# Optimization experiments

Measured on AMD Instinct MI355X. Metric: run time of the kernel, lower is better.

The kernel has to match this reference:

```python
import jax, jax.numpy as jnp
import numpy as np

B, D, E, H = 2048, 1024, 16, 4096
NUM_ACTIVE = 2
LN_EPS = 1e-5
NORM_EPS = 1e-12


def setup_inputs() -> dict:
    key = jax.random.key(0)
    ks = jax.random.split(key, 4)
    s1 = 1.0 / np.sqrt(D)
    s2 = 1.0 / np.sqrt(H)
    return {
        "input": jax.random.normal(ks[0], (B, D), jnp.float32),
        "ln_gamma": jnp.ones((D,), jnp.float32),
        "ln_beta": jnp.zeros((D,), jnp.float32),
        "expert_keys": jax.random.normal(ks[1], (D, E), jnp.float32),
        "W1": jax.random.normal(ks[2], (E, D, H), jnp.float32) * s1,
        "b1": jnp.zeros((E, H), jnp.float32),
        "W2": jax.random.normal(ks[3], (E, H, D), jnp.float32) * s2,
        "b2": jnp.zeros((E, D), jnp.float32),
    }


def reference(input, ln_gamma, ln_beta, expert_keys, W1, b1, W2, b2):
    # Gating: LayerNorm(input) @ normalize(expert_keys, dim=-1)
    mu = jnp.mean(input, axis=-1, keepdims=True)
    var = jnp.mean((input - mu) ** 2, axis=-1, keepdims=True)
    xn = (input - mu) / jnp.sqrt(var + LN_EPS) * ln_gamma + ln_beta
    # F.normalize(expert_keys, dim=-1): each row (per feature) normalized over experts
    keys = expert_keys / jnp.clip(
        jnp.linalg.norm(expert_keys, axis=-1, keepdims=True), NORM_EPS)
    logits = xn @ keys  # [B, E]
    # Top-k routing (argsort descending, take first num_active)
    top_vals, top_ids = jax.lax.top_k(logits, NUM_ACTIVE)  # [B, k]
    gates_k = jax.nn.softmax(top_vals, axis=-1)            # softmax over chosen logits
    gates = jnp.zeros_like(logits).at[
        jnp.arange(logits.shape[0])[:, None], top_ids].set(gates_k)  # [B, E]
    # Experts applied to RAW input (not the normalized gating input), dense-all-experts
    h = jax.nn.relu(jnp.einsum('bd,edh->beh', input, W1) + b1)   # [B, E, H]
    eo = jnp.einsum('beh,ehd->bed', h, W2) + b2                  # [B, E, D]
    # Weighted combine: only top-k experts have nonzero gates
    out = jnp.einsum('bed,be->bd', eo, gates)                    # [B, D]
    return out
```

## Files before the change

kernel.cpp:

```cpp
#include <hip/hip_runtime.h>
#include <hip/hip_bf16.h>
#include <cstdint>
#include <cstddef>

#define D_ 1024
#define H_ 4096
#define E_ 16
#define B_ 2048

constexpr int CAP = 384;

typedef __attribute__((ext_vector_type(4))) float f32x4;
typedef __attribute__((ext_vector_type(8))) short bf16x8;

__device__ __forceinline__ unsigned pack2(float a, float b) {
  __hip_bfloat162 h = __float22bfloat162_rn(make_float2(a, b));
  union { __hip_bfloat162 h2; unsigned u; } cv; cv.h2 = h;
  return cv.u;
}
__device__ __forceinline__ float bflo(unsigned u) { return __uint_as_float(u << 16); }
__device__ __forceinline__ float bfhi(unsigned u) { return __uint_as_float(u & 0xffff0000u); }

#define GLL16(g, l)                                                         \
  __builtin_amdgcn_global_load_lds(                                         \
      (const __attribute__((address_space(1))) void*)(g),                   \
      (__attribute__((address_space(3))) void*)(l), 16, 0, 0)

#define WAITV(n) asm volatile("s_waitcnt vmcnt(" #n ")" ::: "memory")
#define WAITL()  asm volatile("s_waitcnt lgkmcnt(0)" ::: "memory")
#define BAR() __builtin_amdgcn_s_barrier()

__global__ __launch_bounds__(256) void moe_gating3(
    const float* __restrict__ x, const float* __restrict__ gamma,
    const float* __restrict__ beta, const float* __restrict__ keys,
    int* __restrict__ cnt, int4* __restrict__ rmi, float2* __restrict__ rmg,
    unsigned short* __restrict__ xg)
{
  const int b = blockIdx.x, t = threadIdx.x;
  const int w = t >> 6;
  const float4 xv = ((const float4*)(x + (size_t)b * D_))[t];
  float s  = xv.x + xv.y + xv.z + xv.w;
  float sq = xv.x*xv.x + xv.y*xv.y + xv.z*xv.z + xv.w*xv.w;
#pragma unroll
  for (int off = 32; off >= 1; off >>= 1) {
    s  += __shfl_down(s, off);
    sq += __shfl_down(sq, off);
  }
  __shared__ float ssum[4], ssq[4], sstat[2];
  if ((t & 63) == 0) { ssum[w] = s; ssq[w] = sq; }
  __syncthreads();
  if (t == 0) {
    float S = ssum[0] + ssum[1] + ssum[2] + ssum[3];
    float Q = ssq[0] + ssq[1] + ssq[2] + ssq[3];
    float mu  = S * (1.0f / D_);
    float var = Q * (1.0f / D_) - mu * mu;
    sstat[0] = mu; sstat[1] = rsqrtf(var + 1e-5f);
  }
  __syncthreads();
  const float mu = sstat[0], rstd = sstat[1];
  const float4 gv = ((const float4*)gamma)[t];
  const float4 bv = ((const float4*)beta)[t];
  float xn[4] = {(xv.x-mu)*rstd*gv.x+bv.x, (xv.y-mu)*rstd*gv.y+bv.y,
                 (xv.z-mu)*rstd*gv.z+bv.z, (xv.w-mu)*rstd*gv.w+bv.w};
  float acc[E_];
#pragma unroll
  for (int e2 = 0; e2 < E_; ++e2) acc[e2] = 0.f;
#pragma unroll
  for (int j = 0; j < 4; ++j) {
    const int d = 4*t + j;
    const float* kr = keys + (size_t)d * E_;
    float kv[E_];
#pragma unroll
    for (int e2 = 0; e2 < E_; ++e2) kv[e2] = kr[e2];
    float nq = 0.f;
#pragma unroll
    for (int e2 = 0; e2 < E_; ++e2) nq += kv[e2] * kv[e2];
    const float sc = xn[j] / fmaxf(sqrtf(nq), 1e-12f);
#pragma unroll
    for (int e2 = 0; e2 < E_; ++e2) acc[e2] += sc * kv[e2];
  }
#pragma unroll
  for (int off = 1; off < 64; off <<= 1) {
#pragma unroll
    for (int e2 = 0; e2 < E_; ++e2) acc[e2] += __shfl_xor(acc[e2], off);
  }
  __shared__ float wred[4][E_];
  if ((t & 63) == 0) {
#pragma unroll
    for (int e2 = 0; e2 < E_; ++e2) wred[w][e2] = acc[e2];
  }
  __syncthreads();
  __shared__ int sE[2], sP[2];
  if (t == 0) {
    float lg[E_];
#pragma unroll
    for (int e2 = 0; e2 < E_; ++e2)
      lg[e2] = wred[0][e2] + wred[1][e2] + wred[2][e2] + wred[3][e2];
    float v0 = -1e30f; int e0 = 0;
    for (int e2 = 0; e2 < E_; ++e2) { if (lg[e2] > v0) { v0 = lg[e2]; e0 = e2; } }
    float v1 = -1e30f; int e1 = 0;
    for (int e2 = 0; e2 < E_; ++e2) { if (e2 == e0) continue; if (lg[e2] > v1) { v1 = lg[e2]; e1 = e2; } }
    const float g0 = 1.f / (1.f + __expf(v1 - v0));
    const float g1 = 1.f - g0;
    int p0 = atomicAdd(cnt + e0, 1); if (p0 >= CAP) p0 = CAP - 1;
    int p1 = atomicAdd(cnt + e1, 1); if (p1 >= CAP) p1 = CAP - 1;
    rmi[b] = make_int4(e0, p0, e1, p1);
    rmg[b] = make_float2(g0, g1);
    sE[0] = e0; sP[0] = p0;
    sE[1] = e1; sP[1] = p1;
  }
  __syncthreads();
  const uint2 pk = make_uint2(pack2(xv.x, xv.y), pack2(xv.z, xv.w));
#pragma unroll
  for (int i = 0; i < 2; ++i)
    ((uint2*)(xg + ((size_t)sE[i] * CAP + sP[i]) * D_))[t] = pk;
}

template<int KROW, int KLEN, int NTILE, int WN, int SPLITK, bool RELU>
__global__ void __launch_bounds__(256, 3)
moe_gemm(const unsigned short* __restrict__ Asrc, const float* __restrict__ W,
         const float* __restrict__ bias, const int* __restrict__ cnt,
         unsigned short* __restrict__ d0, unsigned short* __restrict__ d1,
         unsigned short* __restrict__ d2, unsigned short* __restrict__ d3)
{
  constexpr int NPHASE = KLEN / 32;
  constexpr int NT = WN / NTILE;
  constexpr int MT = 2;
  constexpr int CF = NTILE / 64;

  const int bx = blockIdx.x;
  const int xcd = bx & 7;
  int slot = bx >> 3;
  const int mt = slot % MT; slot /= MT;
  const int nt = slot % NT; slot /= NT;
  const int eh = slot & 1;
  const int part = slot >> 1;
  const int e  = (xcd << 1) | eh;
  const int nb = nt * NTILE;
  const int koff = part * KLEN;
  unsigned short* dst = (part == 0) ? d0 : (part == 1) ? d1 : (part == 2) ? d2 : d3;

  int cntE = cnt[e]; if (cntE > CAP) cntE = CAP;
  if (mt * 192 >= cntE) return;

  const int t = threadIdx.x, w = t >> 6, lane = t & 63;
  const int l15 = lane & 15, l4 = lane >> 4;

  __shared__ __align__(16) unsigned short As[2][192 * 32];
  __shared__ __align__(16) unsigned short Bs[2][NTILE * 40];

  asm volatile("s_waitcnt vmcnt(0) lgkmcnt(0)" ::: "memory");

  const unsigned short* Ae = Asrc + (size_t)e * CAP * KROW + (size_t)mt * 192 * KROW + koff;
  const float* We = W + (size_t)e * KROW * WN + (size_t)koff * WN + nb;

  const unsigned short *srcA0, *srcA1, *srcA2;
  {
    const int c0 = t,        r0 = c0 >> 2;
    const int c1 = t + 256,  r1 = c1 >> 2;
    const int c2 = t + 512,  r2 = c2 >> 2;
    srcA0 = Ae + (size_t)r0 * KROW + ((c0 & 3) ^ ((r0 >> 1) & 3)) * 8;
    srcA1 = Ae + (size_t)r1 * KROW + ((c1 & 3) ^ ((r1 >> 1) & 3)) * 8;
    srcA2 = Ae + (size_t)r2 * KROW + ((c2 & 3) ^ ((r2 >> 1) & 3)) * 8;
  }
  const float* srcB = We + (size_t)(w * 8) * WN + lane;
  int bofs[CF];
#pragma unroll
  for (int h = 0; h < CF; ++h) {
    const int n = h * 64 + lane;
    bofs[h] = (80 * n + 16 * w) ^ (((n >> 3) & 3) << 4);
  }

#define STAGE(p, BUF) do {                                                  \
    const float* bp_ = srcB + (size_t)(p) * 32 * WN;                        \
    float bl_[CF][8];                                                       \
    _Pragma("unroll")                                                       \
    for (int h = 0; h < CF; ++h)                                            \
      _Pragma("unroll")                                                     \
      for (int j = 0; j < 8; ++j)                                           \
        bl_[h][j] = bp_[(size_t)j * WN + h * 64];                           \
    const int ko_ = (p) * 32;                                               \
    GLL16(srcA0 + ko_, &As[BUF][(0 * 256 + w * 64) * 8]);                   \
    GLL16(srcA1 + ko_, &As[BUF][(1 * 256 + w * 64) * 8]);                   \
    GLL16(srcA2 + ko_, &As[BUF][(2 * 256 + w * 64) * 8]);                   \
    WAITV(3);                                                               \
    _Pragma("unroll")                                                       \
    for (int h = 0; h < CF; ++h) {                                          \
      uint4 q_;                                                             \
      q_.x = pack2(bl_[h][0], bl_[h][1]);                                   \
      q_.y = pack2(bl_[h][2], bl_[h][3]);                                   \
      q_.z = pack2(bl_[h][4], bl_[h][5]);                                   \
      q_.w = pack2(bl_[h][6], bl_[h][7]);                                   \
      *(uint4*)((char*)&Bs[BUF][0] + bofs[h]) = q_;                         \
    }                                                                       \
  } while (0)

  f32x4 acc[12][CF];
#pragma unroll
  for (int rf = 0; rf < 12; ++rf)
#pragma unroll
    for (int cf = 0; cf < CF; ++cf) acc[rf][cf] = f32x4{0,0,0,0};

  const int swA = (l15 >> 1) & 3;
  const int mrow0 = mt * 192;

#define COMP(BUF) do {                                                      \
    bf16x8 BB[CF];                                                          \
    _Pragma("unroll")                                                       \
    for (int cf = 0; cf < CF; ++cf) {                                       \
      const int n_ = w * (16 * CF) + cf * 16 + l15;                         \
      BB[cf] = *(const bf16x8*)((const char*)&Bs[BUF][0]                    \
               + ((80 * n_ + 16 * l4) ^ (((n_ >> 3) & 3) << 4)));           \
    }                                                                       \
    __builtin_amdgcn_s_setprio(1);                                          \
    _Pragma("unroll")                                                       \
    for (int rf = 0; rf < 12; ++rf) {                                       \
      if (mrow0 + rf * 16 < cntE) {                                         \
        const bf16x8 a = *(const bf16x8*)&As[BUF][((rf * 16 + l15) * 4 + (l4 ^ swA)) * 8]; \
        _Pragma("unroll")                                                   \
        for (int cf = 0; cf < CF; ++cf)                                     \
          acc[rf][cf] = __builtin_amdgcn_mfma_f32_16x16x32_bf16(a, BB[cf], acc[rf][cf], 0,0,0); \
      }                                                                     \
    }                                                                       \
    __builtin_amdgcn_s_setprio(0);                                          \
  } while (0)

  STAGE(0, 0);
#pragma unroll 1
  for (int p = 0; p < NPHASE; ++p) {
    if (p + 1 < NPHASE) { STAGE(p + 1, (p + 1) & 1); } else { WAITV(0); }
    WAITL();
    BAR();
    COMP(p & 1);
    BAR();
  }
#undef STAGE
#undef COMP

  unsigned short* dbase = dst + (size_t)e * CAP * WN + nb + w * (16 * CF);
#pragma unroll
  for (int rf = 0; rf < 12; ++rf) {
    if (mrow0 + rf * 16 >= cntE && rf > 0) continue;
#pragma unroll
    for (int cf = 0; cf < CF; ++cf) {
      float bv = 0.f;
      if constexpr (RELU) bv = bias[e * WN + nb + w * (16 * CF) + cf * 16 + l15];
#pragma unroll
      for (int r = 0; r < 4; ++r) {
        const int row = mrow0 + rf * 16 + l4 * 4 + r;
        float v = acc[rf][cf][r];
        if constexpr (RELU) v = fmaxf(v + bv, 0.f);
        const unsigned u01 = pack2(v, __shfl_xor(v, 1));
        const float uo = __shfl_xor(__uint_as_float(u01), 2);
        if ((l15 & 3) == 0)
          *(uint2*)(dbase + (size_t)row * WN + cf * 16 + l15) =
              make_uint2(u01, __float_as_uint(uo));
      }
    }
  }
}

__global__ __launch_bounds__(256) void moe_comb(
    const unsigned short* __restrict__ p0, const unsigned short* __restrict__ p1,
    const unsigned short* __restrict__ p2, const unsigned short* __restrict__ p3,
    const float* __restrict__ b2, const int4* __restrict__ rmi,
    const float2* __restrict__ rmg, float* __restrict__ out)
{
  const int b = blockIdx.x, t = threadIdx.x;
  const int4 m = rmi[b];
  const float2 g = rmg[b];
  const int c = t * 4;
  const size_t offA = ((size_t)m.x * CAP + m.y) * D_ + c;
  const size_t offB = ((size_t)m.z * CAP + m.w) * D_ + c;
  float a0, a1, a2, a3, c0, c1, c2, c3;
  {
    const uint2 ua = *(const uint2*)(p0 + offA);
    const uint2 ub = *(const uint2*)(p0 + offB);
    a0 = bflo(ua.x); a1 = bfhi(ua.x); a2 = bflo(ua.y); a3 = bfhi(ua.y);
    c0 = bflo(ub.x); c1 = bfhi(ub.x); c2 = bflo(ub.y); c3 = bfhi(ub.y);
  }
  const unsigned short* parts[3] = { p1, p2, p3 };
#pragma unroll
  for (int i = 0; i < 3; ++i) {
    if (parts[i] != nullptr) {
      const uint2 ua = *(const uint2*)(parts[i] + offA);
      const uint2 ub = *(const uint2*)(parts[i] + offB);
      a0 += bflo(ua.x); a1 += bfhi(ua.x); a2 += bflo(ua.y); a3 += bfhi(ua.y);
      c0 += bflo(ub.x); c1 += bfhi(ub.x); c2 += bflo(ub.y); c3 += bfhi(ub.y);
    }
  }
  const float4 b2a = *(const float4*)(b2 + (size_t)m.x * D_ + c);
  const float4 b2b = *(const float4*)(b2 + (size_t)m.z * D_ + c);
  float4 o;
  o.x = g.x * (a0 + b2a.x) + g.y * (c0 + b2b.x);
  o.y = g.x * (a1 + b2a.y) + g.y * (c1 + b2b.y);
  o.z = g.x * (a2 + b2a.z) + g.y * (c2 + b2b.z);
  o.w = g.x * (a3 + b2a.w) + g.y * (c3 + b2b.w);
  *(float4*)(out + (size_t)b * D_ + c) = o;
}

extern "C" void kernel_launch(void* const* d_in, const int* in_sizes, int n_in,
                              void* d_out, int out_size, void* d_ws, size_t ws_size,
                              hipStream_t stream) {
  const float* x     = (const float*)d_in[0];
  const float* gamma = (const float*)d_in[1];
  const float* beta  = (const float*)d_in[2];
  const float* keys  = (const float*)d_in[3];
  const float* W1    = (const float*)d_in[4];
  const float* b1    = (const float*)d_in[5];
  const float* W2    = (const float*)d_in[6];
  const float* b2    = (const float*)d_in[7];
  float* out = (float*)d_out;

  char* ws = (char*)d_ws;
  const size_t OFF_RMI = 256;
  const size_t OFF_RMG = OFF_RMI + (size_t)B_ * 16;
  const size_t OFF_XG  = OFF_RMG + (size_t)B_ * 8;
  const size_t EO_SZ   = (size_t)E_ * CAP * D_ * 2;
  const size_t OFF_HW  = OFF_XG + EO_SZ;
  const size_t HW_SZ   = (size_t)E_ * CAP * H_ * 2;
  const size_t OFF_EO1 = OFF_HW + HW_SZ;
  const size_t NEED2   = OFF_EO1 + EO_SZ;
  const size_t NEED4   = OFF_EO1 + 3 * EO_SZ;

  int*    cnt = (int*)ws;
  int4*   rmi = (int4*)(ws + OFF_RMI);
  float2* rmg = (float2*)(ws + OFF_RMG);
  unsigned short* xg  = (unsigned short*)(ws + OFF_XG);
  unsigned short* eo0 = xg;
  unsigned short* hws = (unsigned short*)(ws + OFF_HW);

  (void)hipMemsetAsync(cnt, 0, E_ * sizeof(int), stream);

  moe_gating3<<<B_, 256, 0, stream>>>(x, gamma, beta, keys, cnt, rmi, rmg, xg);

  moe_gemm<D_, D_, 128, H_, 1, true><<<1024, 256, 0, stream>>>(
      xg, W1, b1, cnt, hws, nullptr, nullptr, nullptr);

  if (ws_size >= NEED4) {
    unsigned short* eo1 = (unsigned short*)(ws + OFF_EO1);
    unsigned short* eo2 = (unsigned short*)(ws + OFF_EO1 + EO_SZ);
    unsigned short* eo3 = (unsigned short*)(ws + OFF_EO1 + 2 * EO_SZ);
    moe_gemm<H_, H_ / 4, 128, D_, 4, false><<<1024, 256, 0, stream>>>(
        hws, W2, nullptr, cnt, eo0, eo1, eo2, eo3);
    moe_comb<<<B_, 256, 0, stream>>>(eo0, eo1, eo2, eo3, b2, rmi, rmg, out);
  } else if (ws_size >= NEED2) {
    unsigned short* eo1 = (unsigned short*)(ws + OFF_EO1);
    moe_gemm<H_, H_ / 2, 64, D_, 2, false><<<1024, 256, 0, stream>>>(
        hws, W2, nullptr, cnt, eo0, eo1, nullptr, nullptr);
    moe_comb<<<B_, 256, 0, stream>>>(eo0, eo1, nullptr, nullptr, b2, rmi, rmg, out);
  } else {
    moe_gemm<H_, H_, 64, D_, 1, false><<<512, 256, 0, stream>>>(
        hws, W2, nullptr, cnt, eo0, nullptr, nullptr, nullptr);
    moe_comb<<<B_, 256, 0, stream>>>(eo0, nullptr, nullptr, nullptr, b2, rmi, rmg, out);
  }
}
```

Baseline: 323.6 us.

## Double-buffer B-tile register loads in MoE GEMM and zero counters via kernel

The GEMM main loop now holds two register sets for the fp32 weight tiles and issues the next phase's global loads before converting and writing the current phase's tile to LDS. A partial vmcnt wait lets one phase of loads stay in flight, so global latency can overlap with the bf16 pack and the MFMA work. The loop is unrolled by two with fixed LDS buffers. The hipMemsetAsync for expert counters is replaced by a tiny zeroing kernel to avoid memset launch overhead. The extra register set raises register pressure, and the hardcoded vmcnt values depend on the exact load count per phase.

```diff
diff --git a/kernel.cpp b/kernel.cpp
--- a/kernel.cpp
+++ b/kernel.cpp
@@ -29,6 +29,10 @@
 #define WAITV(n) asm volatile("s_waitcnt vmcnt(" #n ")" ::: "memory")
 #define WAITL()  asm volatile("s_waitcnt lgkmcnt(0)" ::: "memory")
 #define BAR() __builtin_amdgcn_s_barrier()
+
+__global__ void moe_zero(int* __restrict__ cnt) {
+  if (threadIdx.x < E_) cnt[threadIdx.x] = 0;
+}
 
 __global__ __launch_bounds__(256) void moe_gating3(
     const float* __restrict__ x, const float* __restrict__ gamma,
@@ -171,26 +175,33 @@
     bofs[h] = (80 * n + 16 * w) ^ (((n >> 3) & 3) << 4);
   }
 
-#define STAGE(p, BUF) do {                                                  \
+  float R0[CF][8], R1[CF][8];
+
+#define ISSUE(p, Rv, BUF) do {                                              \
     const float* bp_ = srcB + (size_t)(p) * 32 * WN;                        \
-    float bl_[CF][8];                                                       \
     _Pragma("unroll")                                                       \
     for (int h = 0; h < CF; ++h)                                            \
       _Pragma("unroll")                                                     \
       for (int j = 0; j < 8; ++j)                                           \
-        bl_[h][j] = bp_[(size_t)j * WN + h * 64];                           \
+        Rv[h][j] = bp_[(size_t)j * WN + h * 64];                            \
     const int ko_ = (p) * 32;                                               \
     GLL16(srcA0 + ko_, &As[BUF][(0 * 256 + w * 64) * 8]);                   \
     GLL16(srcA1 + ko_, &As[BUF][(1 * 256 + w * 64) * 8]);                   \
     GLL16(srcA2 + ko_, &As[BUF][(2 * 256 + w * 64) * 8]);                   \
-    WAITV(3);                                                               \
+  } while (0)
+
+#define WAIT_OLD() do {                                                     \
+    if constexpr (CF == 2) { WAITV(19); } else { WAITV(11); }               \
+  } while (0)
+
+#define WRITE(Rv, BUF) do {                                                 \
     _Pragma("unroll")                                                       \
     for (int h = 0; h < CF; ++h) {                                          \
       uint4 q_;                                                             \
-      q_.x = pack2(bl_[h][0], bl_[h][1]);                                   \
-      q_.y = pack2(bl_[h][2], bl_[h][3]);                                   \
-      q_.z = pack2(bl_[h][4], bl_[h][5]);                                   \
-      q_.w = pack2(bl_[h][6], bl_[h][7]);                                   \
+      q_.x = pack2(Rv[h][0], Rv[h][1]);                                     \
+      q_.y = pack2(Rv[h][2], Rv[h][3]);                                     \
+      q_.z = pack2(Rv[h][4], Rv[h][5]);                                     \
+      q_.w = pack2(Rv[h][6], Rv[h][7]);                                     \
       *(uint4*)((char*)&Bs[BUF][0] + bofs[h]) = q_;                         \
     }                                                                       \
   } while (0)
@@ -225,16 +236,21 @@
     __builtin_amdgcn_s_setprio(0);                                          \
   } while (0)
 
-  STAGE(0, 0);
+  ISSUE(0, R0, 0);
 #pragma unroll 1
-  for (int p = 0; p < NPHASE; ++p) {
-    if (p + 1 < NPHASE) { STAGE(p + 1, (p + 1) & 1); } else { WAITV(0); }
-    WAITL();
-    BAR();
-    COMP(p & 1);
-    BAR();
-  }
-#undef STAGE
+  for (int p = 0; p < NPHASE; p += 2) {
+    ISSUE(p + 1, R1, 1);
+    WAIT_OLD();
+    WRITE(R0, 0); WAITL(); BAR();
+    COMP(0); BAR();
+    if (p + 2 < NPHASE) { ISSUE(p + 2, R0, 0); WAIT_OLD(); }
+    else { WAITV(0); }
+    WRITE(R1, 1); WAITL(); BAR();
+    COMP(1); BAR();
+  }
+#undef ISSUE
+#undef WAIT_OLD
+#undef WRITE
 #undef COMP
 
   unsigned short* dbase = dst + (size_t)e * CAP * WN + nb + w * (16 * CF);
@@ -330,8 +346,7 @@
   unsigned short* eo0 = xg;
   unsigned short* hws = (unsigned short*)(ws + OFF_HW);
 
-  (void)hipMemsetAsync(cnt, 0, E_ * sizeof(int), stream);
-
+  moe_zero<<<1, 64, 0, stream>>>(cnt);
   moe_gating3<<<B_, 256, 0, stream>>>(x, gamma, beta, keys, cnt, rmi, rmg, xg);
 
   moe_gemm<D_, D_, 128, H_, 1, true><<<1024, 256, 0, stream>>>(
```

Result: faster. 313.1 us (-3.2%).
